# Kernel tuning notes

Hardware: AMD Instinct MI355X
Metric: run time of the kernel (lower is better)

The kernel has to match this reference:

```python
import jax, jax.numpy as jnp
import numpy as np

D = 1024      # input_size / d_model
H = 16        # num_heads
HD = D // H   # head_size = 64
T = 2048      # block_size / seq_len
B = 2
FF = 4 * D
EPS = 1e-5


def setup_inputs() -> dict:
    key = jax.random.key(0)
    ks = jax.random.split(key, 16)
    s_in = 1.0 / np.sqrt(D)
    s_ff = 1.0 / np.sqrt(FF)
    return {
        "x": jax.random.normal(ks[0], (B, T, D), dtype=jnp.float32),
        # per-head unbiased projections, stacked over heads: [H, D, HD]
        "wq": jax.random.normal(ks[1], (H, D, HD), dtype=jnp.float32) * s_in,
        "wk": jax.random.normal(ks[2], (H, D, HD), dtype=jnp.float32) * s_in,
        "wv": jax.random.normal(ks[3], (H, D, HD), dtype=jnp.float32) * s_in,
        "w_proj": jax.random.normal(ks[4], (D, D), dtype=jnp.float32) * s_in,
        "b_proj": jnp.zeros((D,), dtype=jnp.float32),
        "ln1_g": jnp.ones((D,), dtype=jnp.float32),
        "ln1_b": jnp.zeros((D,), dtype=jnp.float32),
        "ln2_g": jnp.ones((D,), dtype=jnp.float32),
        "ln2_b": jnp.zeros((D,), dtype=jnp.float32),
        "w1": jax.random.normal(ks[5], (D, FF), dtype=jnp.float32) * s_in,
        "b1": jnp.zeros((FF,), dtype=jnp.float32),
        "w2": jax.random.normal(ks[6], (FF, D), dtype=jnp.float32) * s_ff,
        "b2": jnp.zeros((D,), dtype=jnp.float32),
    }


def _layernorm(x, g, b):
    mu = jnp.mean(x, axis=-1, keepdims=True)
    var = jnp.mean(jnp.square(x - mu), axis=-1, keepdims=True)
    return (x - mu) * jax.lax.rsqrt(var + EPS) * g + b


def reference(x, wq, wk, wv, w_proj, b_proj, ln1_g, ln1_b, ln2_g, ln2_b, w1, b1, w2, b2):
    Bv, Tv, _ = x.shape
    h = _layernorm(x, ln1_g, ln1_b)                       # [B,T,D]
    q = jnp.einsum("btc,hcd->bhtd", h, wq)
    k = jnp.einsum("btc,hcd->bhtd", h, wk)
    v = jnp.einsum("btc,hcd->bhtd", h, wv)
    scores = jnp.einsum("bhtd,bhsd->bhts", q, k) * (HD ** -0.5)  # [B,H,T,T]
    causal = jnp.tril(jnp.ones((Tv, Tv), dtype=bool))
    scores = jnp.where(causal, scores, -jnp.inf)
    attn = jax.nn.softmax(scores, axis=-1)
    out = jnp.einsum("bhts,bhsd->bhtd", attn, v)          # [B,H,T,HD]
    out = out.transpose(0, 2, 1, 3).reshape(Bv, Tv, H * HD)  # concat heads
    out = out @ w_proj + b_proj
    x = x + out
    h2 = _layernorm(x, ln2_g, ln2_b)
    ff = jax.nn.gelu(h2 @ w1 + b1, approximate=False) @ w2 + b2
    return x + ff
```

## Files before the change

### kernel.cpp

```cpp
#include <hip/hip_runtime.h>
#include <hip/hip_bf16.h>
#include <cstdint>
#include <cstddef>
#include <math.h>

#define D_ 1024
#define H_ 16
#define HD_ 64
#define T_ 2048
#define B_ 2
#define FF_ 4096
#define BT_ (B_*T_)
#define NT_ 32

typedef unsigned short u16;
typedef __attribute__((ext_vector_type(8))) __bf16 bf16x8;
typedef __attribute__((ext_vector_type(8))) u16 u16x8;
typedef __attribute__((ext_vector_type(4))) float f32x4;

__device__ __forceinline__ u16 f2bf(float f) {
  unsigned u = __builtin_bit_cast(unsigned, f);
  u += 0x7FFFu + ((u >> 16) & 1u);
  return (u16)(u >> 16);
}

__device__ __forceinline__ unsigned cvt_pk_bf16(float a, float b) {
  unsigned r;
  asm("v_cvt_pk_bf16_f32 %0, %1, %2" : "=v"(r) : "v"(a), "v"(b));
  return r;
}

__device__ __forceinline__ void gload16(const void* g, void* l) {
  __builtin_amdgcn_global_load_lds((__attribute__((address_space(1))) void*)g,
                                   (__attribute__((address_space(3))) void*)l, 16, 0, 0);
}

__global__ __launch_bounds__(256) void transpose_all(
    const float* __restrict__ wq, const float* __restrict__ wk,
    const float* __restrict__ wv, const float* __restrict__ w_proj,
    const float* __restrict__ w1, const float* __restrict__ w2,
    u16* __restrict__ wqkv_t, u16* __restrict__ wproj_t,
    u16* __restrict__ w1t, u16* __restrict__ w2t) {
  __shared__ float tile[32][33];
  const int bid = blockIdx.x;
  const float* in; u16* out; int R, C, tx, ty;
  if (bid < 3072) {
    const int w = bid >> 10, rem = bid & 1023;
    const int z = rem >> 6, t = rem & 63;
    tx = t & 1; ty = t >> 1;
    R = D_; C = HD_;
    in  = (w == 0 ? wq : w == 1 ? wk : wv) + (size_t)z * R * C;
    out = wqkv_t + (size_t)w * D_ * D_ + (size_t)z * C * R;
  } else if (bid < 4096) {
    const int t = bid - 3072;
    tx = t & 31; ty = t >> 5;
    R = D_; C = D_; in = w_proj; out = wproj_t;
  } else if (bid < 8192) {
    const int t = bid - 4096;
    tx = t & 127; ty = t >> 7;
    R = D_; C = FF_; in = w1; out = w1t;
  } else {
    const int t = bid - 8192;
    tx = t & 31; ty = t >> 5;
    R = FF_; C = D_; in = w2; out = w2t;
  }
  const int x = tx * 32 + threadIdx.x;
  const int y0 = ty * 32 + threadIdx.y;
  #pragma unroll
  for (int j = 0; j < 32; j += 8)
    tile[threadIdx.y + j][threadIdx.x] = in[(size_t)(y0 + j) * C + x];
  __syncthreads();
  const int orr = ty * 32 + threadIdx.x;
  const int oc0 = tx * 32 + threadIdx.y;
  #pragma unroll
  for (int j = 0; j < 32; j += 8)
    out[(size_t)(oc0 + j) * R + orr] = f2bf(tile[threadIdx.x][threadIdx.y + j]);
}

__global__ __launch_bounds__(256) void ln_rows(const float* __restrict__ x,
    const float* __restrict__ g, const float* __restrict__ bb, u16* __restrict__ out) {
  const int row = blockIdx.x, tid = threadIdx.x;
  const float4 v = ((const float4*)(x + (size_t)row * D_))[tid];
  float s = v.x + v.y + v.z + v.w;
  float sq = v.x*v.x + v.y*v.y + v.z*v.z + v.w*v.w;
  #pragma unroll
  for (int m = 1; m < 64; m <<= 1) { s += __shfl_xor(s, m); sq += __shfl_xor(sq, m); }
  __shared__ float ss[4], qs[4];
  if ((tid & 63) == 0) { ss[tid >> 6] = s; qs[tid >> 6] = sq; }
  __syncthreads();
  s  = ss[0] + ss[1] + ss[2] + ss[3];
  sq = qs[0] + qs[1] + qs[2] + qs[3];
  const float mean = s * (1.f / D_);
  const float var  = sq * (1.f / D_) - mean * mean;
  const float rstd = rsqrtf(var + 1e-5f);
  const float4 gv = ((const float4*)g)[tid];
  const float4 bv = ((const float4*)bb)[tid];
  u16 o[4];
  o[0] = f2bf((v.x - mean) * rstd * gv.x + bv.x);
  o[1] = f2bf((v.y - mean) * rstd * gv.y + bv.y);
  o[2] = f2bf((v.z - mean) * rstd * gv.z + bv.z);
  o[3] = f2bf((v.w - mean) * rstd * gv.w + bv.w);
  *(ushort4*)(out + (size_t)row * D_ + tid * 4) = *(ushort4*)o;
}

template<int ACT, int BIAS, int OUTBF, int PARTIAL, int QKVE>
__global__ __launch_bounds__(256, 4) void gemm128(
    const u16* __restrict__ A, const u16* __restrict__ Bt,
    const float* __restrict__ bias, const float* resid,
    void* Cout, int M, int N, int K, int Kper) {
  __shared__ __attribute__((aligned(16))) u16 LA[2][128 * 32];
  __shared__ __attribute__((aligned(16))) u16 LB[2][128 * 32];

  const int tid = threadIdx.x;
  const int wid = tid >> 6, lane = tid & 63;
  const int wr = wid >> 1, wc = wid & 1;
  const int frow = lane & 15, hi = lane >> 4;

  const int gx = gridDim.x;
  const int nwg = gx * gridDim.y;
  const int orig = blockIdx.y * gx + blockIdx.x;
  const int cpx = nwg >> 3;
  const int swz = (orig & 7) * cpx + (orig >> 3);
  const int bm = (swz / gx) * 128, bn = (swz % gx) * 128;
  const int z = PARTIAL ? blockIdx.z : 0;
  const int koff = z * Kper;
  const int nt = Kper >> 5;

  const int srow = tid >> 2;
  const int gch  = (tid & 3) ^ (srow & 3);
  const u16* Ag0 = A + (size_t)(bm + srow) * K + koff + gch * 8;
  const u16* Ag1 = Ag0 + (size_t)64 * K;
  const u16* Bg0 = Bt + (size_t)(bn + srow) * K + koff + gch * 8;
  const u16* Bg1 = Bg0 + (size_t)64 * K;
  const int ldsA0 = (wid * 16) * 32, ldsA1 = (64 + wid * 16) * 32;

  f32x4 acc[4][4] = {};

  #define STAGE32(kt, db)                              \
    {                                                  \
      const int ko = (kt) * 32;                        \
      gload16(Ag0 + ko, &LA[db][ldsA0]);               \
      gload16(Ag1 + ko, &LA[db][ldsA1]);               \
      gload16(Bg0 + ko, &LB[db][ldsA0]);               \
      gload16(Bg1 + ko, &LB[db][ldsA1]);               \
    }

  STAGE32(0, 0);

  for (int t = 0; t < nt; ++t) {
    const int db = t & 1;
    if (t + 1 < nt) {
      STAGE32(t + 1, db ^ 1);
      asm volatile("s_waitcnt vmcnt(4)" ::: "memory");
    } else {
      asm volatile("s_waitcnt vmcnt(0)" ::: "memory");
    }
    __builtin_amdgcn_s_barrier();

    const u16* Ab = &LA[db][0];
    const u16* Bb = &LB[db][0];

    bf16x8 af[4], bfr[4];
    #pragma unroll
    for (int i = 0; i < 4; i++) {
      const int ra = wr * 64 + i * 16 + frow;
      af[i]  = *(const bf16x8*)(Ab + ra * 32 + ((hi ^ (ra & 3)) << 3));
      const int rb = wc * 64 + i * 16 + frow;
      bfr[i] = *(const bf16x8*)(Bb + rb * 32 + ((hi ^ (rb & 3)) << 3));
    }
    __builtin_amdgcn_s_setprio(1);
    #pragma unroll
    for (int mi = 0; mi < 4; mi++)
      #pragma unroll
      for (int ni = 0; ni < 4; ni++)
        acc[mi][ni] = __builtin_amdgcn_mfma_f32_16x16x32_bf16(af[mi], bfr[ni], acc[mi][ni], 0, 0, 0);
    __builtin_amdgcn_s_setprio(0);
    __builtin_amdgcn_s_barrier();
  }
  #undef STAGE32

  const int r0 = bm + wr * 64 + hi * 4;
  const int c0 = bn + wc * 64 + frow;
  #pragma unroll
  for (int mi = 0; mi < 4; mi++) {
    #pragma unroll
    for (int ni = 0; ni < 4; ni++) {
      #pragma unroll
      for (int r = 0; r < 4; r++) {
        float v = acc[mi][ni][r];
        const int rr = r0 + mi * 16 + r;
        const int cc = c0 + ni * 16;
        if (QKVE) {
          const int region = bn >> 10;
          u16* qo = (u16*)Cout;
          u16* ko = qo + (size_t)4 * 1024 * 1024;
          u16* vo = qo + (size_t)8 * 1024 * 1024;
          const int c1 = cc & 1023;
          const int h = c1 >> 6, d = c1 & 63;
          const int bb2 = rr >> 11, t2 = rr & 2047;
          const int bh = bb2 * 16 + h;
          if (region == 0)
            qo[((size_t)bh * T_ + t2) * HD_ + d] = f2bf(v * 0.18033688011112042f);
          else if (region == 1)
            ko[((size_t)bh * T_ + t2) * HD_ + d] = f2bf(v);
          else
            vo[((size_t)bh * HD_ + d) * T_ + t2] = f2bf(v);
        } else if (PARTIAL) {
          ((float*)Cout)[((size_t)z * M + rr) * N + cc] = v;
        } else {
          if (BIAS) v += bias[cc];
          if (ACT == 1) {
            const float u = v * (0.79788456f + 0.03567740814f * v * v);
            const float e = exp2f(fminf(u * 2.885390082f, 80.f));
            v = v - v * __builtin_amdgcn_rcpf(1.0f + e);
          }
          if (resid) v += resid[(size_t)rr * N + cc];
          if (OUTBF) ((u16*)Cout)[(size_t)rr * N + cc] = f2bf(v);
          else       ((float*)Cout)[(size_t)rr * N + cc] = v;
        }
      }
    }
  }
}

template<int NPART>
__global__ __launch_bounds__(256) void reduce_parts(
    const float* __restrict__ parts, const float* __restrict__ bias,
    const float* __restrict__ resid, float* __restrict__ out, int MN, int N) {
  const int i4 = (blockIdx.x * 256 + threadIdx.x) * 4;
  if (i4 >= MN) return;
  float4 s = *(const float4*)(parts + i4);
  #pragma unroll
  for (int p = 1; p < NPART; p++) {
    const float4 t = *(const float4*)(parts + (size_t)p * MN + i4);
    s.x += t.x; s.y += t.y; s.z += t.z; s.w += t.w;
  }
  const float4 bv = *(const float4*)(bias + (i4 & (N - 1)));
  const float4 rv = *(const float4*)(resid + i4);
  s.x += bv.x + rv.x; s.y += bv.y + rv.y; s.z += bv.z + rv.z; s.w += bv.w + rv.w;
  *(float4*)(out + i4) = s;
}

__global__ __launch_bounds__(256) void reduce2_ln(
    const float* __restrict__ parts, const float* __restrict__ bias,
    const float* __restrict__ resid, const float* __restrict__ g,
    const float* __restrict__ bb, float* __restrict__ xout,
    u16* __restrict__ h2, int MN) {
  const int row = blockIdx.x, tid = threadIdx.x;
  const int i4 = row * D_ + tid * 4;
  float4 s = *(const float4*)(parts + i4);
  const float4 t = *(const float4*)(parts + (size_t)MN + i4);
  const float4 bv = *(const float4*)(bias + tid * 4);
  const float4 rv = *(const float4*)(resid + i4);
  s.x += t.x + bv.x + rv.x; s.y += t.y + bv.y + rv.y;
  s.z += t.z + bv.z + rv.z; s.w += t.w + bv.w + rv.w;
  *(float4*)(xout + i4) = s;
  float sm = s.x + s.y + s.z + s.w;
  float sq = s.x*s.x + s.y*s.y + s.z*s.z + s.w*s.w;
  #pragma unroll
  for (int m = 1; m < 64; m <<= 1) { sm += __shfl_xor(sm, m); sq += __shfl_xor(sq, m); }
  __shared__ float ss[4], qs[4];
  if ((tid & 63) == 0) { ss[tid >> 6] = sm; qs[tid >> 6] = sq; }
  __syncthreads();
  sm = ss[0] + ss[1] + ss[2] + ss[3];
  sq = qs[0] + qs[1] + qs[2] + qs[3];
  const float mean = sm * (1.f / D_);
  const float var  = sq * (1.f / D_) - mean * mean;
  const float rstd = rsqrtf(var + 1e-5f);
  const float4 gv = ((const float4*)g)[tid];
  const float4 b2v = ((const float4*)bb)[tid];
  u16 o[4];
  o[0] = f2bf((s.x - mean) * rstd * gv.x + b2v.x);
  o[1] = f2bf((s.y - mean) * rstd * gv.y + b2v.y);
  o[2] = f2bf((s.z - mean) * rstd * gv.z + b2v.z);
  o[3] = f2bf((s.w - mean) * rstd * gv.w + b2v.w);
  *(ushort4*)(h2 + (size_t)row * D_ + tid * 4) = *(ushort4*)o;
}

__global__ __launch_bounds__(256, 2) void attn_fwd(
    const u16* __restrict__ q, const u16* __restrict__ k,
    const u16* __restrict__ vt, u16* __restrict__ out) {
  __shared__ __attribute__((aligned(16))) u16 Ps[4][16 * 64];
  __shared__ __attribute__((aligned(16))) u16 Kb[2][64 * 64];
  __shared__ __attribute__((aligned(16))) u16 Vb[2][64 * 64];

  const int bid = blockIdx.x;
  const int xcd = bid & 7, j = bid >> 3;
  const int bh  = xcd + 8 * (j & 3);
  const int qp  = j >> 2;
  const int b = bh >> 4, h = bh & 15;
  const int tid = threadIdx.x, wid = tid >> 6, lane = tid & 63;
  const u16* kh = k  + (size_t)bh * T_ * HD_;
  const u16* vh = vt + (size_t)bh * HD_ * T_;

  const int frow = lane & 15;
  const int hi   = lane >> 4;
  const int fk   = hi * 8;
  const int rowb = hi * 4;
  const int colb = frow;
  const int srow = tid >> 3;
  const int gch  = (tid & 7) ^ (srow & 7);

  u16x8 onebits = (u16x8)((u16)0x3F80);
  bf16x8 b_one = (frow == 0) ? __builtin_bit_cast(bf16x8, onebits) : (bf16x8){};

  u16* Pw = &Ps[wid][0];

  for (int qi = 0; qi < 2; ++qi) {
    const int qb = qi ? (31 - qp) : qp;
    const int q0 = qb * 64;
    const int nkt = qb + 1;

    const u16* qrow = q + ((size_t)bh * T_ + q0 + wid * 16 + frow) * HD_;
    bf16x8 aq[2];
    aq[0] = *(const bf16x8*)(qrow + fk);
    aq[1] = *(const bf16x8*)(qrow + 32 + fk);

    float m2[4] = {-3e38f, -3e38f, -3e38f, -3e38f};
    f32x4 acc_l = {};
    f32x4 acc_o[4] = {};

    int cur = 0;
    #pragma unroll
    for (int p = 0; p < 2; p++) {
      gload16(kh + (size_t)(p * 32 + srow) * HD_ + gch * 8, &Kb[0][(p * 32 + wid * 8) * 64]);
      gload16(vh + (size_t)(p * 32 + srow) * T_ + gch * 8,  &Vb[0][(p * 32 + wid * 8) * 64]);
    }
    __syncthreads();

    for (int kt = 0; kt < nkt; ++kt) {
      if (kt + 1 < nkt) {
        const int nx = cur ^ 1, ktn = kt + 1;
        #pragma unroll
        for (int p = 0; p < 2; p++) {
          gload16(kh + (size_t)(ktn * 64 + p * 32 + srow) * HD_ + gch * 8,
                  &Kb[nx][(p * 32 + wid * 8) * 64]);
          gload16(vh + (size_t)(p * 32 + srow) * T_ + ktn * 64 + gch * 8,
                  &Vb[nx][(p * 32 + wid * 8) * 64]);
        }
      }

      const u16* Kc = &Kb[cur][0];
      const u16* Vc = &Vb[cur][0];

      float p2[4][4];
      __builtin_amdgcn_s_setprio(1);
      #pragma unroll
      for (int ni = 0; ni < 4; ni++) {
        f32x4 s = {};
        #pragma unroll
        for (int ks = 0; ks < 2; ks++) {
          const int row = ni * 16 + frow;
          const int ch  = ks * 4 + hi;
          bf16x8 bk = *(const bf16x8*)(Kc + row * 64 + ((ch ^ (row & 7)) << 3));
          s = __builtin_amdgcn_mfma_f32_16x16x32_bf16(aq[ks], bk, s, 0, 0, 0);
        }
        #pragma unroll
        for (int r = 0; r < 4; r++) p2[ni][r] = s[r];
      }
      __builtin_amdgcn_s_setprio(0);

      if (kt == nkt - 1) {
        #pragma unroll
        for (int ni = 0; ni < 4; ni++)
          #pragma unroll
          for (int r = 0; r < 4; r++) {
            const bool msk = (ni * 16 + colb) > (wid * 16 + rowb + r);
            if (msk) p2[ni][r] = -3e38f;
          }
      }

      float lmax[4];
      #pragma unroll
      for (int r = 0; r < 4; r++)
        lmax[r] = fmaxf(fmaxf(p2[0][r], p2[1][r]), fmaxf(p2[2][r], p2[3][r]));
      int ok = 1;
      #pragma unroll
      for (int r = 0; r < 4; r++) ok &= (lmax[r] <= m2[r] + 8.0f);
      if (!__all(ok)) {
        #pragma unroll
        for (int r = 0; r < 4; r++) {
          float rm = lmax[r];
          rm = fmaxf(rm, __shfl_xor(rm, 1));
          rm = fmaxf(rm, __shfl_xor(rm, 2));
          rm = fmaxf(rm, __shfl_xor(rm, 4));
          rm = fmaxf(rm, __shfl_xor(rm, 8));
          const float mnew = fmaxf(m2[r], rm);
          const float corr = exp2f(m2[r] - mnew);
          m2[r] = mnew;
          acc_l[r] *= corr;
          #pragma unroll
          for (int ni = 0; ni < 4; ni++) acc_o[ni][r] *= corr;
        }
      }
      #pragma unroll
      for (int ni = 0; ni < 4; ni++)
        #pragma unroll
        for (int r = 0; r < 4; r++) p2[ni][r] = exp2f(p2[ni][r] - m2[r]);

      #pragma unroll
      for (int ni = 0; ni < 4; ni++) {
        #pragma unroll
        for (int r = 0; r < 4; r += 2) {
          const unsigned pk = cvt_pk_bf16(p2[ni][r], p2[ni][r + 1]);
          const int lr0 = rowb + r, lr1 = rowb + r + 1;
          const int ch = ni * 2 + (colb >> 3);
          Pw[lr0 * 64 + ((ch ^ (lr0 & 7)) << 3) + (colb & 7)] = (u16)pk;
          Pw[lr1 * 64 + ((ch ^ (lr1 & 7)) << 3) + (colb & 7)] = (u16)(pk >> 16);
        }
      }
      bf16x8 ap[2];
      {
        const int c0 = (0 * 4 + hi) ^ (frow & 7);
        const int c1 = (1 * 4 + hi) ^ (frow & 7);
        ap[0] = *(const bf16x8*)(Pw + frow * 64 + (c0 << 3));
        ap[1] = *(const bf16x8*)(Pw + frow * 64 + (c1 << 3));
      }

      __builtin_amdgcn_s_setprio(1);
      #pragma unroll
      for (int ks = 0; ks < 2; ks++)
        acc_l = __builtin_amdgcn_mfma_f32_16x16x32_bf16(ap[ks], b_one, acc_l, 0, 0, 0);
      #pragma unroll
      for (int ni = 0; ni < 4; ni++) {
        #pragma unroll
        for (int ks = 0; ks < 2; ks++) {
          const int row = ni * 16 + frow;
          const int ch  = ks * 4 + hi;
          bf16x8 bv = *(const bf16x8*)(Vc + row * 64 + ((ch ^ (row & 7)) << 3));
          acc_o[ni] = __builtin_amdgcn_mfma_f32_16x16x32_bf16(ap[ks], bv, acc_o[ni], 0, 0, 0);
        }
      }
      __builtin_amdgcn_s_setprio(0);

      __syncthreads();
      cur ^= 1;
    }

    float linv[4];
    #pragma unroll
    for (int r = 0; r < 4; r++) {
      const float lv = __shfl(acc_l[r], lane & 48);
      linv[r] = 1.0f / lv;
    }
    #pragma unroll
    for (int ni = 0; ni < 4; ni++)
      #pragma unroll
      for (int r = 0; r < 4; r++) {
        const float ov = acc_o[ni][r] * linv[r];
        const size_t row = (size_t)b * T_ + q0 + wid * 16 + rowb + r;
        out[row * D_ + h * HD_ + ni * 16 + colb] = f2bf(ov);
      }
  }
}

extern "C" void kernel_launch(void* const* d_in, const int* in_sizes, int n_in,
                              void* d_out, int out_size, void* d_ws, size_t ws_size,
                              hipStream_t stream) {
  (void)in_sizes; (void)n_in; (void)out_size; (void)ws_size;
  const float* x      = (const float*)d_in[0];
  const float* wq     = (const float*)d_in[1];
  const float* wk     = (const float*)d_in[2];
  const float* wv     = (const float*)d_in[3];
  const float* w_proj = (const float*)d_in[4];
  const float* b_proj = (const float*)d_in[5];
  const float* ln1_g  = (const float*)d_in[6];
  const float* ln1_b  = (const float*)d_in[7];
  const float* ln2_g  = (const float*)d_in[8];
  const float* ln2_b  = (const float*)d_in[9];
  const float* w1     = (const float*)d_in[10];
  const float* b1     = (const float*)d_in[11];
  const float* w2     = (const float*)d_in[12];
  const float* b2     = (const float*)d_in[13];

  uint8_t* ws = (uint8_t*)d_ws;
  const size_t MB = 1024 * 1024;
  u16* wqkv_t = (u16*)(ws + 0);
  u16* wproj_t = (u16*)(ws + 6 * MB);
  u16* w1t  = (u16*)(ws + 8 * MB);
  u16* w2t  = (u16*)(ws + 16 * MB);
  u16* hbuf = (u16*)(ws + 24 * MB);
  u16* qb   = (u16*)(ws + 56 * MB);
  u16* kb   = (u16*)(ws + 64 * MB);
  u16* vtb  = (u16*)(ws + 72 * MB);
  u16* aout = (u16*)(ws + 80 * MB);
  u16* h2   = (u16*)(ws + 88 * MB);
  u16* ff1  = (u16*)(ws + 96 * MB);
  float* pparts = (float*)(ws + 32 * MB);
  float* fparts = (float*)(ws + 32 * MB);
  float* xout = (float*)d_out;

  transpose_all<<<12288, dim3(32, 8), 0, stream>>>(
      wq, wk, wv, w_proj, w1, w2, wqkv_t, wproj_t, w1t, w2t);

  ln_rows<<<BT_, 256, 0, stream>>>(x, ln1_g, ln1_b, hbuf);

  gemm128<0,0,0,0,1><<<dim3(3072/128, BT_/128), 256, 0, stream>>>(
      hbuf, wqkv_t, nullptr, nullptr, qb, BT_, 3072, D_, D_);

  attn_fwd<<<dim3(512), 256, 0, stream>>>(qb, kb, vtb, aout);

  gemm128<0,0,0,1,0><<<dim3(D_/128, BT_/128, 2), 256, 0, stream>>>(
      aout, wproj_t, nullptr, nullptr, pparts, BT_, D_, D_, D_/2);
  reduce2_ln<<<BT_, 256, 0, stream>>>(
      pparts, b_proj, x, ln2_g, ln2_b, xout, h2, BT_*D_);

  gemm128<1,1,1,0,0><<<dim3(FF_/128, BT_/128), 256, 0, stream>>>(
      h2, w1t, b1, nullptr, ff1, BT_, FF_, D_, D_);

  gemm128<0,0,0,1,0><<<dim3(D_/128, BT_/128, 4), 256, 0, stream>>>(
      ff1, w2t, nullptr, nullptr, fparts, BT_, D_, FF_, FF_/4);
  reduce_parts<4><<<(BT_*D_)/1024, 256, 0, stream>>>(
      fparts, b2, xout, xout, BT_*D_, D_);
}
```

Before: 246.3 us.

## Compute transposed S in attention to keep P in registers via lane shuffles

Measured after the change: 248.7 us. No clear change (+1.0%).

```diff
diff --git a/kernel.cpp b/kernel.cpp
--- a/kernel.cpp
+++ b/kernel.cpp
@@ -17,6 +17,7 @@
 typedef __attribute__((ext_vector_type(8))) __bf16 bf16x8;
 typedef __attribute__((ext_vector_type(8))) u16 u16x8;
 typedef __attribute__((ext_vector_type(4))) float f32x4;
+typedef __attribute__((ext_vector_type(4))) unsigned u32x4;
 
 __device__ __forceinline__ u16 f2bf(float f) {
   unsigned u = __builtin_bit_cast(unsigned, f);
@@ -280,7 +281,6 @@
 __global__ __launch_bounds__(256, 2) void attn_fwd(
     const u16* __restrict__ q, const u16* __restrict__ k,
     const u16* __restrict__ vt, u16* __restrict__ out) {
-  __shared__ __attribute__((aligned(16))) u16 Ps[4][16 * 64];
   __shared__ __attribute__((aligned(16))) u16 Kb[2][64 * 64];
   __shared__ __attribute__((aligned(16))) u16 Vb[2][64 * 64];
 
@@ -297,14 +297,8 @@
   const int hi   = lane >> 4;
   const int fk   = hi * 8;
   const int rowb = hi * 4;
-  const int colb = frow;
   const int srow = tid >> 3;
   const int gch  = (tid & 7) ^ (srow & 7);
-
-  u16x8 onebits = (u16x8)((u16)0x3F80);
-  bf16x8 b_one = (frow == 0) ? __builtin_bit_cast(bf16x8, onebits) : (bf16x8){};
-
-  u16* Pw = &Ps[wid][0];
 
   for (int qi = 0; qi < 2; ++qi) {
     const int qb = qi ? (31 - qp) : qp;
@@ -316,8 +310,8 @@
     aq[0] = *(const bf16x8*)(qrow + fk);
     aq[1] = *(const bf16x8*)(qrow + 32 + fk);
 
-    float m2[4] = {-3e38f, -3e38f, -3e38f, -3e38f};
-    f32x4 acc_l = {};
+    float m2 = -3e38f;
+    float acc_l = 0.f;
     f32x4 acc_o[4] = {};
 
     int cur = 0;
@@ -343,7 +337,7 @@
       const u16* Kc = &Kb[cur][0];
       const u16* Vc = &Vb[cur][0];
 
-      float p2[4][4];
+      f32x4 p2[4];
       __builtin_amdgcn_s_setprio(1);
       #pragma unroll
       for (int ni = 0; ni < 4; ni++) {
@@ -353,10 +347,9 @@
           const int row = ni * 16 + frow;
           const int ch  = ks * 4 + hi;
           bf16x8 bk = *(const bf16x8*)(Kc + row * 64 + ((ch ^ (row & 7)) << 3));
-          s = __builtin_amdgcn_mfma_f32_16x16x32_bf16(aq[ks], bk, s, 0, 0, 0);
-        }
-        #pragma unroll
-        for (int r = 0; r < 4; r++) p2[ni][r] = s[r];
+          s = __builtin_amdgcn_mfma_f32_16x16x32_bf16(bk, aq[ks], s, 0, 0, 0);
+        }
+        p2[ni] = s;
       }
       __builtin_amdgcn_s_setprio(0);
 
@@ -364,63 +357,62 @@
         #pragma unroll
         for (int ni = 0; ni < 4; ni++)
           #pragma unroll
-          for (int r = 0; r < 4; r++) {
-            const bool msk = (ni * 16 + colb) > (wid * 16 + rowb + r);
-            if (msk) p2[ni][r] = -3e38f;
-          }
-      }
-
-      float lmax[4];
-      #pragma unroll
-      for (int r = 0; r < 4; r++)
-        lmax[r] = fmaxf(fmaxf(p2[0][r], p2[1][r]), fmaxf(p2[2][r], p2[3][r]));
-      int ok = 1;
-      #pragma unroll
-      for (int r = 0; r < 4; r++) ok &= (lmax[r] <= m2[r] + 8.0f);
-      if (!__all(ok)) {
+          for (int r = 0; r < 4; r++)
+            if ((ni * 16 + rowb + r) > (wid * 16 + frow)) p2[ni][r] = -3e38f;
+      }
+
+      float lm = fmaxf(fmaxf(p2[0][0], p2[0][1]), fmaxf(p2[0][2], p2[0][3]));
+      #pragma unroll
+      for (int ni = 1; ni < 4; ni++)
+        lm = fmaxf(lm, fmaxf(fmaxf(p2[ni][0], p2[ni][1]), fmaxf(p2[ni][2], p2[ni][3])));
+      if (!__all(lm <= m2 + 8.0f)) {
+        float rm = lm;
+        rm = fmaxf(rm, __shfl_xor(rm, 16));
+        rm = fmaxf(rm, __shfl_xor(rm, 32));
+        const float mnew = fmaxf(m2, rm);
+        const float corr = exp2f(m2 - mnew);
+        m2 = mnew;
+        acc_l *= corr;
         #pragma unroll
         for (int r = 0; r < 4; r++) {
-          float rm = lmax[r];
-          rm = fmaxf(rm, __shfl_xor(rm, 1));
-          rm = fmaxf(rm, __shfl_xor(rm, 2));
-          rm = fmaxf(rm, __shfl_xor(rm, 4));
-          rm = fmaxf(rm, __shfl_xor(rm, 8));
-          const float mnew = fmaxf(m2[r], rm);
-          const float corr = exp2f(m2[r] - mnew);
-          m2[r] = mnew;
-          acc_l[r] *= corr;
+          const float cr = __shfl(corr, (lane & 48) | (rowb + r));
           #pragma unroll
-          for (int ni = 0; ni < 4; ni++) acc_o[ni][r] *= corr;
-        }
-      }
+          for (int ni = 0; ni < 4; ni++) acc_o[ni][r] *= cr;
+        }
+      }
+      float ls = 0.f;
       #pragma unroll
       for (int ni = 0; ni < 4; ni++)
         #pragma unroll
-        for (int r = 0; r < 4; r++) p2[ni][r] = exp2f(p2[ni][r] - m2[r]);
-
+        for (int r = 0; r < 4; r++) {
+          const float e = exp2f(p2[ni][r] - m2);
+          p2[ni][r] = e;
+          ls += e;
+        }
+      acc_l += ls;
+
+      unsigned pk[4][2];
       #pragma unroll
       for (int ni = 0; ni < 4; ni++) {
-        #pragma unroll
-        for (int r = 0; r < 4; r += 2) {
-          const unsigned pk = cvt_pk_bf16(p2[ni][r], p2[ni][r + 1]);
-          const int lr0 = rowb + r, lr1 = rowb + r + 1;
-          const int ch = ni * 2 + (colb >> 3);
-          Pw[lr0 * 64 + ((ch ^ (lr0 & 7)) << 3) + (colb & 7)] = (u16)pk;
-          Pw[lr1 * 64 + ((ch ^ (lr1 & 7)) << 3) + (colb & 7)] = (u16)(pk >> 16);
-        }
+        pk[ni][0] = cvt_pk_bf16(p2[ni][0], p2[ni][1]);
+        pk[ni][1] = cvt_pk_bf16(p2[ni][2], p2[ni][3]);
       }
       bf16x8 ap[2];
-      {
-        const int c0 = (0 * 4 + hi) ^ (frow & 7);
-        const int c1 = (1 * 4 + hi) ^ (frow & 7);
-        ap[0] = *(const bf16x8*)(Pw + frow * 64 + (c0 << 3));
-        ap[1] = *(const bf16x8*)(Pw + frow * 64 + (c1 << 3));
+      #pragma unroll
+      for (int ks = 0; ks < 2; ks++) {
+        u32x4 wv4;
+        #pragma unroll
+        for (int w = 0; w < 4; w++) {
+          const int hi_s = ((hi & 1) << 1) | (w >> 1);
+          const int srcl = (lane & 15) | (hi_s << 4);
+          const unsigned lo = (unsigned)__shfl((int)pk[2 * ks][w & 1], srcl);
+          const unsigned hi2 = (unsigned)__shfl((int)pk[2 * ks + 1][w & 1], srcl);
+          wv4[w] = (hi & 2) ? hi2 : lo;
+        }
+        ap[ks] = __builtin_bit_cast(bf16x8, wv4);
       }
 
       __builtin_amdgcn_s_setprio(1);
-      #pragma unroll
-      for (int ks = 0; ks < 2; ks++)
-        acc_l = __builtin_amdgcn_mfma_f32_16x16x32_bf16(ap[ks], b_one, acc_l, 0, 0, 0);
       #pragma unroll
       for (int ni = 0; ni < 4; ni++) {
         #pragma unroll
@@ -437,20 +429,19 @@
       cur ^= 1;
     }
 
-    float linv[4];
+    acc_l += __shfl_xor(acc_l, 16);
+    acc_l += __shfl_xor(acc_l, 32);
+    const float linv_q = 1.0f / acc_l;
     #pragma unroll
     for (int r = 0; r < 4; r++) {
-      const float lv = __shfl(acc_l[r], lane & 48);
-      linv[r] = 1.0f / lv;
-    }
-    #pragma unroll
-    for (int ni = 0; ni < 4; ni++)
-      #pragma unroll
-      for (int r = 0; r < 4; r++) {
-        const float ov = acc_o[ni][r] * linv[r];
+      const float lr = __shfl(linv_q, (lane & 48) | (rowb + r));
+      #pragma unroll
+      for (int ni = 0; ni < 4; ni++) {
+        const float ov = acc_o[ni][r] * lr;
         const size_t row = (size_t)b * T_ + q0 + wid * 16 + rowb + r;
-        out[row * D_ + h * HD_ + ni * 16 + colb] = f2bf(ov);
-      }
+        out[row * D_ + h * HD_ + ni * 16 + frow] = f2bf(ov);
+      }
+    }
   }
 }
 
```
